# Performance work log

Hardware: AMD Instinct MI355X
Metric: run time of the kernel (lower is better)

Reference implementation:

```python
import jax, jax.numpy as jnp
import numpy as np

B, S, D, H = 4, 2048, 1024, 16
HD = D // H
QMIN, QMAX = -128.0, 127.0


def fq(x):
    """Int8 per-tensor fake-quant (quantize-dequantize), straight-through."""
    s = jnp.maximum(jnp.max(jnp.abs(x)) / QMAX, 1e-8)
    q = jnp.clip(jnp.round(x / s), QMIN, QMAX) * s
    return x + jax.lax.stop_gradient(q - x)


def layernorm(x, g, b):
    m = jnp.mean(x, axis=-1, keepdims=True)
    v = jnp.var(x, axis=-1, keepdims=True)
    return (x - m) * jax.lax.rsqrt(v + 1e-5) * g + b


def rope(x):
    # x: [B, H, S, HD]; rotate-half RoPE
    half = HD // 2
    inv = 1.0 / (10000.0 ** (jnp.arange(half, dtype=jnp.float32) / half))
    ang = jnp.arange(S, dtype=jnp.float32)[:, None] * inv[None, :]  # [S, half]
    cos, sin = jnp.cos(ang), jnp.sin(ang)
    x1, x2 = x[..., :half], x[..., half:]
    return jnp.concatenate([x1 * cos - x2 * sin, x1 * sin + x2 * cos], axis=-1)


def setup_inputs() -> dict:
    key = jax.random.key(0)
    ks = jax.random.split(key, 16)
    w = lambda k, shp: jax.random.normal(k, shp, dtype=jnp.float32) * 0.02
    return {
        "x": jax.random.normal(ks[0], (B, S, D), dtype=jnp.float32),
        "g1": jnp.ones((D,), jnp.float32), "bn1": jnp.zeros((D,), jnp.float32),
        "Wq": w(ks[1], (D, D)), "bq": jnp.zeros((D,), jnp.float32),
        "Wk": w(ks[2], (D, D)), "bk": jnp.zeros((D,), jnp.float32),
        "Wv": w(ks[3], (D, D)), "bv": jnp.zeros((D,), jnp.float32),
        "Wo": w(ks[4], (D, D)), "bo": jnp.zeros((D,), jnp.float32),
        "g2": jnp.ones((D,), jnp.float32), "bn2": jnp.zeros((D,), jnp.float32),
        "W1": w(ks[5], (4 * D, D)), "bf1": jnp.zeros((4 * D,), jnp.float32),
        "W2": w(ks[6], (D, 4 * D)), "bf2": jnp.zeros((D,), jnp.float32),
    }


def reference(x, g1, bn1, Wq, bq, Wk, bk, Wv, bv, Wo, bo, g2, bn2, W1, bf1, W2, bf2):
    # --- attention branch: LN -> int8 quant -> RoPE MHSA -> quant add ---
    residual = x
    h = fq(layernorm(x, g1, bn1))  # post_norm1_quant
    q = h @ fq(Wq).T + bq
    k = h @ fq(Wk).T + bk
    v = h @ fq(Wv).T + bv
    q = rope(q.reshape(B, S, H, HD).transpose(0, 2, 1, 3))
    k = rope(k.reshape(B, S, H, HD).transpose(0, 2, 1, 3))
    v = v.reshape(B, S, H, HD).transpose(0, 2, 1, 3)
    scores = jnp.einsum("bhqd,bhkd->bhqk", q, k) / np.sqrt(HD).astype(np.float32)
    attn = jax.nn.softmax(scores, axis=-1)
    o = jnp.einsum("bhqk,bhkd->bhqd", attn, v)
    o = o.transpose(0, 2, 1, 3).reshape(B, S, D)
    o = fq(o @ fq(Wo).T + bo)  # attn returns quant tensor
    x = fq(o + residual)       # QuantAdd
    # --- MLP branch: LN -> quant -> fc1 -> GELU -> quant -> fc2 -> quant add ---
    residual = x
    h = fq(layernorm(x, g2, bn2))  # post_norm2_quant
    h = h @ fq(W1).T + bf1
    h = jax.nn.gelu(h, approximate=False)
    h = fq(h)                       # post_gelu_quant
    h = h @ fq(W2).T + bf2
    return fq(h + residual)         # QuantAdd
```

## Files before the change

### kernel.cpp

```cpp
#include <hip/hip_runtime.h>
#include <math.h>

#define Bdim 4
#define Sdim 2048
#define Ddim 1024
#define Hdim 16
#define HDdim 64

typedef unsigned long long u64;
typedef unsigned short ushort_t;
typedef int int4v __attribute__((ext_vector_type(4)));
typedef short short8v __attribute__((ext_vector_type(8)));
typedef float float4v __attribute__((ext_vector_type(4)));
typedef unsigned short us4v __attribute__((ext_vector_type(4)));

__device__ __forceinline__ float qdq_f(float x, float amax) {
  float s = fmaxf(amax / 127.0f, 1e-8f);
  float r = rintf(x / s);
  r = fminf(fmaxf(r, -128.0f), 127.0f);
  return r * s;
}

__device__ __forceinline__ void atomicMaxF(float* a, float v) {
  atomicMax((int*)a, __float_as_int(v));
}

__device__ __forceinline__ float blockMax256(float v) {
  __shared__ float sred[4];
  #pragma unroll
  for (int o = 32; o > 0; o >>= 1) v = fmaxf(v, __shfl_xor(v, o));
  if ((threadIdx.x & 63) == 0) sred[threadIdx.x >> 6] = v;
  __syncthreads();
  return fmaxf(fmaxf(sred[0], sred[1]), fmaxf(sred[2], sred[3]));
}

__device__ __forceinline__ ushort_t f2bf(float f) {
  unsigned u = __float_as_uint(f);
  return (ushort_t)((u + 0x7FFFu + ((u >> 16) & 1u)) >> 16);
}
__device__ __forceinline__ float bf2f(ushort_t h) {
  return __uint_as_float(((unsigned)h) << 16);
}

__global__ void init_scalars(float* s) { s[threadIdx.x] = 0.0f; }

__global__ void bcat_kernel(const float* __restrict__ bq, const float* __restrict__ bk,
                            const float* __restrict__ bv, float* __restrict__ o) {
  int t = blockIdx.x * 256 + threadIdx.x;
  o[t] = (t < 1024) ? bq[t] : (t < 2048) ? bk[t - 1024] : bv[t - 2048];
}

__global__ __launch_bounds__(256) void absmax6_kernel(
    const float* __restrict__ Wq, const float* __restrict__ Wk,
    const float* __restrict__ Wv, const float* __restrict__ Wo,
    const float* __restrict__ W1, const float* __restrict__ W2,
    float* __restrict__ Sc)
{
  const u64 DD = (u64)Ddim * Ddim;
  int blk = blockIdx.x;
  const float* src; float* dst; u64 lb, nb, n;
  if (blk < 256)       { src = Wq; dst = Sc + 1; lb = blk;        nb = 256;  n = DD; }
  else if (blk < 512)  { src = Wk; dst = Sc + 2; lb = blk - 256;  nb = 256;  n = DD; }
  else if (blk < 768)  { src = Wv; dst = Sc + 3; lb = blk - 512;  nb = 256;  n = DD; }
  else if (blk < 1024) { src = Wo; dst = Sc + 4; lb = blk - 768;  nb = 256;  n = DD; }
  else if (blk < 2048) { src = W1; dst = Sc + 5; lb = blk - 1024; nb = 1024; n = 4 * DD; }
  else                 { src = W2; dst = Sc + 6; lb = blk - 2048; nb = 1024; n = 4 * DD; }
  u64 i = lb * 256 + threadIdx.x;
  u64 stride = nb * 256;
  float m = 0.0f;
  for (; i < n; i += stride) m = fmaxf(m, fabsf(src[i]));
  m = blockMax256(m);
  if (threadIdx.x == 0) atomicMaxF(dst, m);
}

__global__ __launch_bounds__(256) void quantw_kernel(
    const float* __restrict__ Wq, const float* __restrict__ Wk,
    const float* __restrict__ Wv, const float* __restrict__ Wo,
    const float* __restrict__ W1, const float* __restrict__ W2,
    signed char* __restrict__ Wq8, signed char* __restrict__ Wk8,
    signed char* __restrict__ Wv8, ushort_t* __restrict__ WoBF,
    signed char* __restrict__ W18, signed char* __restrict__ W28,
    const float* __restrict__ Sc)
{
  const u64 DD = (u64)Ddim * Ddim;
  int blk = blockIdx.x;
  if (blk < 2816) {
    const float* src; signed char* dst; float sa; u64 lb, nb, n4;
    if (blk < 256)       { src = Wq; dst = Wq8; sa = Sc[1]; lb = blk;        nb = 256;  n4 = DD / 4; }
    else if (blk < 512)  { src = Wk; dst = Wk8; sa = Sc[2]; lb = blk - 256;  nb = 256;  n4 = DD / 4; }
    else if (blk < 768)  { src = Wv; dst = Wv8; sa = Sc[3]; lb = blk - 512;  nb = 256;  n4 = DD / 4; }
    else if (blk < 1792) { src = W1; dst = W18; sa = Sc[5]; lb = blk - 768;  nb = 1024; n4 = DD; }
    else                 { src = W2; dst = W28; sa = Sc[6]; lb = blk - 1792; nb = 1024; n4 = DD; }
    const float is = 1.0f / fmaxf(sa / 127.0f, 1e-8f);
    u64 i = lb * 256 + threadIdx.x;
    u64 stride = nb * 256;
    for (; i < n4; i += stride) {
      float4 v = ((const float4*)src)[i];
      int b0 = (int)fminf(fmaxf(rintf(v.x * is), -128.0f), 127.0f) & 255;
      int b1 = (int)fminf(fmaxf(rintf(v.y * is), -128.0f), 127.0f) & 255;
      int b2 = (int)fminf(fmaxf(rintf(v.z * is), -128.0f), 127.0f) & 255;
      int b3 = (int)fminf(fmaxf(rintf(v.w * is), -128.0f), 127.0f) & 255;
      ((unsigned*)dst)[i] = (unsigned)(b0 | (b1 << 8) | (b2 << 16) | (b3 << 24));
    }
  } else {
    const float is = 1.0f / fmaxf(Sc[4] / 127.0f, 1e-8f);
    u64 i = (u64)(blk - 2816) * 256 + threadIdx.x;
    u64 stride = 1024ull * 256;
    for (; i < DD; i += stride) {
      float r = fminf(fmaxf(rintf(Wo[i] * is), -128.0f), 127.0f);
      WoBF[i] = f2bf(r);
    }
  }
}

__global__ __launch_bounds__(256) void quant8_kernel(
    const float* __restrict__ x, const float* __restrict__ amaxp,
    signed char* __restrict__ q, u64 n4)
{
  const float is = 1.0f / fmaxf(*amaxp / 127.0f, 1e-8f);
  u64 i = (u64)blockIdx.x * 256 + threadIdx.x;
  u64 stride = (u64)gridDim.x * 256;
  for (; i < n4; i += stride) {
    float4 v = ((const float4*)x)[i];
    int b0 = (int)fminf(fmaxf(rintf(v.x * is), -128.0f), 127.0f) & 255;
    int b1 = (int)fminf(fmaxf(rintf(v.y * is), -128.0f), 127.0f) & 255;
    int b2 = (int)fminf(fmaxf(rintf(v.z * is), -128.0f), 127.0f) & 255;
    int b3 = (int)fminf(fmaxf(rintf(v.w * is), -128.0f), 127.0f) & 255;
    ((unsigned*)q)[i] = (unsigned)(b0 | (b1 << 8) | (b2 << 16) | (b3 << 24));
  }
}

__global__ __launch_bounds__(256) void ln_kernel(
    const float* __restrict__ x, const float* __restrict__ g,
    const float* __restrict__ beta, const float* __restrict__ inAmax,
    float* __restrict__ y, float* __restrict__ amaxOut)
{
  __shared__ float sred[4];
  __shared__ float smv[2];
  const int tid = threadIdx.x;
  const u64 row = blockIdx.x;
  const float* xr = x + row * Ddim;
  float* yr = y + row * Ddim;
  float aIn = inAmax ? *inAmax : 0.0f;

  float vals[4];
  float sum = 0.0f;
  #pragma unroll
  for (int i = 0; i < 4; i++) {
    float v = xr[tid + (i << 8)];
    if (inAmax) v = qdq_f(v, aIn);
    vals[i] = v;
    sum += v;
  }
  #pragma unroll
  for (int o = 32; o > 0; o >>= 1) sum += __shfl_xor(sum, o);
  if ((tid & 63) == 0) sred[tid >> 6] = sum;
  __syncthreads();
  if (tid == 0) smv[0] = (sred[0] + sred[1] + sred[2] + sred[3]) * (1.0f / 1024.0f);
  __syncthreads();
  const float mean = smv[0];

  float dev = 0.0f;
  #pragma unroll
  for (int i = 0; i < 4; i++) { float d = vals[i] - mean; dev += d * d; }
  #pragma unroll
  for (int o = 32; o > 0; o >>= 1) dev += __shfl_xor(dev, o);
  if ((tid & 63) == 0) sred[tid >> 6] = dev;
  __syncthreads();
  if (tid == 0) {
    float var = (sred[0] + sred[1] + sred[2] + sred[3]) * (1.0f / 1024.0f);
    smv[1] = 1.0f / sqrtf(var + 1e-5f);
  }
  __syncthreads();
  const float inv = smv[1];

  float lmax = 0.0f;
  #pragma unroll
  for (int i = 0; i < 4; i++) {
    int c = tid + (i << 8);
    float ov = (vals[i] - mean) * inv * g[c] + beta[c];
    yr[c] = ov;
    lmax = fmaxf(lmax, fabsf(ov));
  }
  #pragma unroll
  for (int o = 32; o > 0; o >>= 1) lmax = fmaxf(lmax, __shfl_xor(lmax, o));
  __syncthreads();
  if ((tid & 63) == 0) sred[tid >> 6] = lmax;
  __syncthreads();
  if (tid == 0)
    atomicMaxF(amaxOut, fmaxf(fmaxf(sred[0], sred[1]), fmaxf(sred[2], sred[3])));
}

template <int EPI>
__global__ __launch_bounds__(256) void gemm_i8(
    const signed char* __restrict__ A8, const signed char* __restrict__ B8,
    const float* __restrict__ bias, float* __restrict__ C,
    int M, int N, int K,
    const float* __restrict__ sAp, const float* __restrict__ sBp,
    float* __restrict__ amaxOut,
    const float* __restrict__ Tm = nullptr,
    const float* __restrict__ amaxT = nullptr)
{
  __shared__ __align__(16) signed char As[128][80];
  __shared__ __align__(16) signed char Bs[128][80];
  const int tid = threadIdx.x;
  const int wave = tid >> 6, lane = tid & 63;
  const int quad = lane >> 4, l16 = lane & 15;
  const int wy = wave >> 1, wx = wave & 1;
  const int m0 = blockIdx.y << 7, n0 = blockIdx.x << 7;
  const float sA = fmaxf(*sAp / 127.0f, 1e-8f);
  const float sB = fmaxf(*sBp / 127.0f, 1e-8f);
  const float sAB = sA * sB;
  const float aT = (EPI == 2) ? *amaxT : 0.0f;

  const int sr = tid >> 2;
  const int sc = (tid & 3) << 4;

  int4v acc[4][4] = {};
  for (int k0 = 0; k0 < K; k0 += 64) {
    #pragma unroll
    for (int p = 0; p < 2; p++) {
      int r = sr + (p << 6);
      uint4 av = *(const uint4*)&A8[(u64)(m0 + r) * K + k0 + sc];
      uint4 bv = *(const uint4*)&B8[(u64)(n0 + r) * K + k0 + sc];
      *(uint4*)&As[r][sc] = av;
      *(uint4*)&Bs[r][sc] = bv;
    }
    __syncthreads();
    int4v af[4], bf[4];
    #pragma unroll
    for (int mt = 0; mt < 4; mt++)
      af[mt] = *(const int4v*)&As[(wy << 6) + (mt << 4) + l16][quad << 4];
    #pragma unroll
    for (int nt = 0; nt < 4; nt++)
      bf[nt] = *(const int4v*)&Bs[(wx << 6) + (nt << 4) + l16][quad << 4];
    #pragma unroll
    for (int mt = 0; mt < 4; mt++)
      #pragma unroll
      for (int nt = 0; nt < 4; nt++)
        acc[mt][nt] = __builtin_amdgcn_mfma_i32_16x16x64_i8(af[mt], bf[nt], acc[mt][nt], 0, 0, 0);
    __syncthreads();
  }

  float lmax = 0.0f;
  #pragma unroll
  for (int mt = 0; mt < 4; mt++) {
    #pragma unroll
    for (int reg = 0; reg < 4; reg++) {
      int row = m0 + (wy << 6) + (mt << 4) + (quad << 2) + reg;
      #pragma unroll
      for (int nt = 0; nt < 4; nt++) {
        int col = n0 + (wx << 6) + (nt << 4) + l16;
        float v = (float)acc[mt][nt][reg] * sAB + bias[col];
        if (EPI == 1) {
          v = 0.5f * v * (1.0f + erff(v * 0.70710678118654752440f));
          lmax = fmaxf(lmax, fabsf(v));
        }
        if (EPI == 2) {
          v += qdq_f(Tm[(u64)row * N + col], aT);
          lmax = fmaxf(lmax, fabsf(v));
        }
        C[(u64)row * N + col] = v;
      }
    }
  }
  if (EPI >= 1) {
    lmax = blockMax256(lmax);
    if (tid == 0) atomicMaxF(amaxOut, lmax);
  }
}

__global__ __launch_bounds__(256) void gemm_qkv3(
    const signed char* __restrict__ A8, const signed char* __restrict__ B8,
    const float* __restrict__ bias, float* __restrict__ C,
    const float* __restrict__ Sc)
{
  __shared__ __align__(16) signed char As[128][80];
  __shared__ __align__(16) signed char Bs[128][80];
  const int tid = threadIdx.x;
  const int wave = tid >> 6, lane = tid & 63;
  const int quad = lane >> 4, l16 = lane & 15;
  const int wy = wave >> 1, wx = wave & 1;
  const int m0 = blockIdx.y << 7, n0 = blockIdx.x << 7;
  const int K = Ddim, N = 3 * Ddim;
  const int seg = n0 >> 10;
  const float sA = fmaxf(Sc[0] / 127.0f, 1e-8f);
  const float sB = fmaxf(Sc[1 + seg] / 127.0f, 1e-8f);
  const float sAB = sA * sB;

  const int sr = tid >> 2;
  const int sc_ = (tid & 3) << 4;

  int4v acc[4][4] = {};
  for (int k0 = 0; k0 < K; k0 += 64) {
    #pragma unroll
    for (int p = 0; p < 2; p++) {
      int r = sr + (p << 6);
      uint4 av = *(const uint4*)&A8[(u64)(m0 + r) * K + k0 + sc_];
      uint4 bv = *(const uint4*)&B8[(u64)(n0 + r) * K + k0 + sc_];
      *(uint4*)&As[r][sc_] = av;
      *(uint4*)&Bs[r][sc_] = bv;
    }
    __syncthreads();
    int4v af[4], bf[4];
    #pragma unroll
    for (int mt = 0; mt < 4; mt++)
      af[mt] = *(const int4v*)&As[(wy << 6) + (mt << 4) + l16][quad << 4];
    #pragma unroll
    for (int nt = 0; nt < 4; nt++)
      bf[nt] = *(const int4v*)&Bs[(wx << 6) + (nt << 4) + l16][quad << 4];
    #pragma unroll
    for (int mt = 0; mt < 4; mt++)
      #pragma unroll
      for (int nt = 0; nt < 4; nt++)
        acc[mt][nt] = __builtin_amdgcn_mfma_i32_16x16x64_i8(af[mt], bf[nt], acc[mt][nt], 0, 0, 0);
    __syncthreads();
  }

  #pragma unroll
  for (int mt = 0; mt < 4; mt++) {
    #pragma unroll
    for (int reg = 0; reg < 4; reg++) {
      int row = m0 + (wy << 6) + (mt << 4) + (quad << 2) + reg;
      #pragma unroll
      for (int nt = 0; nt < 4; nt++) {
        int col = n0 + (wx << 6) + (nt << 4) + l16;
        C[(u64)row * N + col] = (float)acc[mt][nt][reg] * sAB + bias[col];
      }
    }
  }
}

__global__ __launch_bounds__(256) void gemm_bf16_wo(
    const ushort_t* __restrict__ Ahi, const ushort_t* __restrict__ Alo,
    const ushort_t* __restrict__ Bw, const float* __restrict__ bias,
    float* __restrict__ C, int M, int N, int K,
    const float* __restrict__ sWp, float* __restrict__ amaxOut)
{
  __shared__ __align__(16) ushort_t Hs[128][40];
  __shared__ __align__(16) ushort_t Ls[128][40];
  __shared__ __align__(16) ushort_t Ws[128][40];
  const int tid = threadIdx.x;
  const int wave = tid >> 6, lane = tid & 63;
  const int quad = lane >> 4, l16 = lane & 15;
  const int wy = wave >> 1, wx = wave & 1;
  const int m0 = blockIdx.y << 7, n0 = blockIdx.x << 7;
  const float sW = fmaxf(*sWp / 127.0f, 1e-8f);

  const int sr = tid >> 2;
  const int sce = (tid & 3) << 3;

  float4v acc[4][4] = {};
  for (int k0 = 0; k0 < K; k0 += 32) {
    #pragma unroll
    for (int p = 0; p < 2; p++) {
      int r = sr + (p << 6);
      uint4 hv = *(const uint4*)&Ahi[(u64)(m0 + r) * K + k0 + sce];
      uint4 lv = *(const uint4*)&Alo[(u64)(m0 + r) * K + k0 + sce];
      uint4 wv = *(const uint4*)&Bw[(u64)(n0 + r) * K + k0 + sce];
      *(uint4*)&Hs[r][sce] = hv;
      *(uint4*)&Ls[r][sce] = lv;
      *(uint4*)&Ws[r][sce] = wv;
    }
    __syncthreads();
    short8v ah[4], al[4], bw[4];
    #pragma unroll
    for (int mt = 0; mt < 4; mt++) {
      ah[mt] = *(const short8v*)&Hs[(wy << 6) + (mt << 4) + l16][quad << 3];
      al[mt] = *(const short8v*)&Ls[(wy << 6) + (mt << 4) + l16][quad << 3];
    }
    #pragma unroll
    for (int nt = 0; nt < 4; nt++)
      bw[nt] = *(const short8v*)&Ws[(wx << 6) + (nt << 4) + l16][quad << 3];
    #pragma unroll
    for (int mt = 0; mt < 4; mt++)
      #pragma unroll
      for (int nt = 0; nt < 4; nt++) {
        acc[mt][nt] = __builtin_amdgcn_mfma_f32_16x16x32_bf16(ah[mt], bw[nt], acc[mt][nt], 0, 0, 0);
        acc[mt][nt] = __builtin_amdgcn_mfma_f32_16x16x32_bf16(al[mt], bw[nt], acc[mt][nt], 0, 0, 0);
      }
    __syncthreads();
  }

  float lmax = 0.0f;
  #pragma unroll
  for (int mt = 0; mt < 4; mt++) {
    #pragma unroll
    for (int reg = 0; reg < 4; reg++) {
      int row = m0 + (wy << 6) + (mt << 4) + (quad << 2) + reg;
      #pragma unroll
      for (int nt = 0; nt < 4; nt++) {
        int col = n0 + (wx << 6) + (nt << 4) + l16;
        float v = acc[mt][nt][reg] * sW + bias[col];
        lmax = fmaxf(lmax, fabsf(v));
        C[(u64)row * N + col] = v;
      }
    }
  }
  lmax = blockMax256(lmax);
  if (tid == 0) atomicMaxF(amaxOut, lmax);
}

__global__ __launch_bounds__(256) void prep_attn(
    const float* __restrict__ QKV,
    ushort_t* __restrict__ QH, ushort_t* __restrict__ QL,
    ushort_t* __restrict__ KH, ushort_t* __restrict__ KL,
    ushort_t* __restrict__ VTH, ushort_t* __restrict__ VTL,
    float* __restrict__ NQ, float* __restrict__ KMX)
{
  const int bh = blockIdx.y;
  const int b = bh >> 4, h = bh & 15;
  const int s0 = blockIdx.x << 6;
  const int tid = threadIdx.x;
  float kml = 0.0f;

  #pragma unroll
  for (int i = 0; i < 8; i++) {
    int idx = tid + (i << 8);
    int s = idx >> 5, hp = idx & 31;
    int sa = s0 + s;
    u64 gin = (u64)(b * Sdim + sa) * 3072 + (h << 6) + hp;
    float inv = powf(10000.0f, -(float)hp * (1.0f / 32.0f));
    float ang = (float)sa * inv;
    float cs = cosf(ang), sn = sinf(ang);
    float q1 = QKV[gin],        q2 = QKV[gin + 32];
    float k1 = QKV[gin + 1024], k2 = QKV[gin + 1056];
    float qo1 = (q1 * cs - q2 * sn) * 0.125f;
    float qo2 = (q1 * sn + q2 * cs) * 0.125f;
    float ko1 = k1 * cs - k2 * sn;
    float ko2 = k1 * sn + k2 * cs;
    u64 go = ((u64)bh * Sdim + sa) * HDdim + hp;
    ushort_t t;
    t = f2bf(qo1); QH[go]      = t; QL[go]      = f2bf(qo1 - bf2f(t));
    t = f2bf(qo2); QH[go + 32] = t; QL[go + 32] = f2bf(qo2 - bf2f(t));
    t = f2bf(ko1); KH[go]      = t; KL[go]      = f2bf(ko1 - bf2f(t));
    t = f2bf(ko2); KH[go + 32] = t; KL[go + 32] = f2bf(ko2 - bf2f(t));
    float nq2 = qo1 * qo1 + qo2 * qo2;
    float nk2 = ko1 * ko1 + ko2 * ko2;
    #pragma unroll
    for (int o = 16; o >= 1; o >>= 1) {
      nq2 += __shfl_xor(nq2, o);
      nk2 += __shfl_xor(nk2, o);
    }
    if (hp == 0) {
      NQ[(u64)bh * Sdim + sa] = sqrtf(nq2);
      kml = fmaxf(kml, sqrtf(nk2));
    }
  }
  kml = blockMax256(kml);
  if (tid == 0) atomicMaxF(&KMX[bh], kml);

  __shared__ ushort_t VHs[64][66], VLs[64][66];
  #pragma unroll
  for (int i = 0; i < 4; i++) {
    int idx4 = tid + (i << 8);
    int s = idx4 >> 4, c4 = (idx4 & 15) << 2;
    u64 gin = (u64)(b * Sdim + s0 + s) * 3072 + 2048 + (h << 6) + c4;
    float4 vv = *(const float4*)&QKV[gin];
    float va[4] = {vv.x, vv.y, vv.z, vv.w};
    #pragma unroll
    for (int j = 0; j < 4; j++) {
      ushort_t vh = f2bf(va[j]);
      VHs[s][c4 + j] = vh;
      VLs[s][c4 + j] = f2bf(va[j] - bf2f(vh));
    }
  }
  __syncthreads();
  #pragma unroll
  for (int i = 0; i < 4; i++) {
    int idx4 = tid + (i << 8);
    int hd = idx4 >> 4, s4 = (idx4 & 15) << 2;
    us4v oh, ol;
    #pragma unroll
    for (int j = 0; j < 4; j++) { oh[j] = VHs[s4 + j][hd]; ol[j] = VLs[s4 + j][hd]; }
    u64 go = ((u64)bh * HDdim + hd) * Sdim + s0 + s4;
    *(us4v*)&VTH[go] = oh;
    *(us4v*)&VTL[go] = ol;
  }
}

__global__ __launch_bounds__(256) void attn_kernel(
    const ushort_t* __restrict__ QH, const ushort_t* __restrict__ QL,
    const ushort_t* __restrict__ KH, const ushort_t* __restrict__ KL,
    const ushort_t* __restrict__ VTH, const ushort_t* __restrict__ VTL,
    const float* __restrict__ NQ, const float* __restrict__ KMX,
    ushort_t* __restrict__ OHI, ushort_t* __restrict__ OLO)
{
  __shared__ __align__(16) ushort_t KHs[64][72], KLs[64][72];
  __shared__ __align__(16) ushort_t VHs[64][72], VLs[64][72];
  __shared__ __align__(16) float PF[128][68];
  const int tid = threadIdx.x;
  const int wave = tid >> 6, lane = tid & 63;
  const int quad = lane >> 4, l16 = lane & 15;
  const int w32 = wave << 5;
  const int bh = blockIdx.y;
  const int b = bh >> 4, h = bh & 15;
  const int q0 = blockIdx.x << 7;
  const u64 bhS = (u64)bh * Sdim;

  short8v qh[2][2], ql[2][2];
  #pragma unroll
  for (int mt = 0; mt < 2; mt++)
    #pragma unroll
    for (int kk = 0; kk < 2; kk++) {
      u64 g = (bhS + q0 + w32 + (mt << 4) + l16) * HDdim + (kk << 5) + (quad << 3);
      qh[mt][kk] = *(const short8v*)&QH[g];
      ql[mt][kk] = *(const short8v*)&QL[g];
    }

  const float kmax = KMX[bh] * 1.0009765625f;
  float Mb[2][4], lsum[2][4];
  #pragma unroll
  for (int mt = 0; mt < 2; mt++)
    #pragma unroll
    for (int r = 0; r < 4; r++) {
      Mb[mt][r] = NQ[bhS + q0 + w32 + (mt << 4) + (quad << 2) + r] * kmax;
      lsum[mt][r] = 0.0f;
    }

  float4v oacc[2][4] = {};

  for (int j0 = 0; j0 < Sdim; j0 += 64) {
    __syncthreads();
    #pragma unroll
    for (int i = 0; i < 2; i++) {
      int idx = tid + (i << 8);
      int r = idx >> 3, c8 = (idx & 7) << 3;
      u64 gk = (bhS + j0 + r) * HDdim + c8;
      *(uint4*)&KHs[r][c8] = *(const uint4*)&KH[gk];
      *(uint4*)&KLs[r][c8] = *(const uint4*)&KL[gk];
      u64 gv = ((u64)bh * HDdim + r) * Sdim + j0 + c8;
      *(uint4*)&VHs[r][c8] = *(const uint4*)&VTH[gv];
      *(uint4*)&VLs[r][c8] = *(const uint4*)&VTL[gv];
    }
    __syncthreads();

    float4v sc[2][4] = {};
    #pragma unroll
    for (int kk = 0; kk < 2; kk++)
      #pragma unroll
      for (int nt = 0; nt < 4; nt++) {
        short8v bh_ = *(const short8v*)&KHs[(nt << 4) + l16][(kk << 5) + (quad << 3)];
        short8v bl_ = *(const short8v*)&KLs[(nt << 4) + l16][(kk << 5) + (quad << 3)];
        #pragma unroll
        for (int mt = 0; mt < 2; mt++) {
          sc[mt][nt] = __builtin_amdgcn_mfma_f32_16x16x32_bf16(qh[mt][kk], bh_, sc[mt][nt], 0, 0, 0);
          sc[mt][nt] = __builtin_amdgcn_mfma_f32_16x16x32_bf16(qh[mt][kk], bl_, sc[mt][nt], 0, 0, 0);
          sc[mt][nt] = __builtin_amdgcn_mfma_f32_16x16x32_bf16(ql[mt][kk], bh_, sc[mt][nt], 0, 0, 0);
        }
      }

    #pragma unroll
    for (int mt = 0; mt < 2; mt++)
      #pragma unroll
      for (int r = 0; r < 4; r++) {
        int prow = w32 + (mt << 4) + (quad << 2) + r;
        float lacc = 0.0f;
        #pragma unroll
        for (int nt = 0; nt < 4; nt++) {
          float p = __expf(sc[mt][nt][r] - Mb[mt][r]);
          lacc += p;
          PF[prow][(nt << 4) + l16] = p;
        }
        lsum[mt][r] += lacc;
      }

    #pragma unroll
    for (int kk = 0; kk < 2; kk++) {
      short8v vh[4], vl[4];
      #pragma unroll
      for (int nt = 0; nt < 4; nt++) {
        vh[nt] = *(const short8v*)&VHs[(nt << 4) + l16][(kk << 5) + (quad << 3)];
        vl[nt] = *(const short8v*)&VLs[(nt << 4) + l16][(kk << 5) + (quad << 3)];
      }
      #pragma unroll
      for (int mt = 0; mt < 2; mt++) {
        const float* prp = &PF[w32 + (mt << 4) + l16][(kk << 5) + (quad << 3)];
        float4v pa = *(const float4v*)prp;
        float4v pb = *(const float4v*)(prp + 4);
        short8v ph, pl;
        #pragma unroll
        for (int j = 0; j < 4; j++) {
          unsigned ua = __float_as_uint(pa[j]);
          unsigned ub = __float_as_uint(pb[j]);
          float la = pa[j] - __uint_as_float(ua & 0xffff0000u);
          float lb = pb[j] - __uint_as_float(ub & 0xffff0000u);
          ph[j]     = (short)(ua >> 16);
          ph[4 + j] = (short)(ub >> 16);
          pl[j]     = (short)(__float_as_uint(la) >> 16);
          pl[4 + j] = (short)(__float_as_uint(lb) >> 16);
        }
        #pragma unroll
        for (int nt = 0; nt < 4; nt++) {
          oacc[mt][nt] = __builtin_amdgcn_mfma_f32_16x16x32_bf16(ph, vh[nt], oacc[mt][nt], 0, 0, 0);
          oacc[mt][nt] = __builtin_amdgcn_mfma_f32_16x16x32_bf16(ph, vl[nt], oacc[mt][nt], 0, 0, 0);
          oacc[mt][nt] = __builtin_amdgcn_mfma_f32_16x16x32_bf16(pl, vh[nt], oacc[mt][nt], 0, 0, 0);
        }
      }
    }
  }

  #pragma unroll
  for (int mt = 0; mt < 2; mt++)
    #pragma unroll
    for (int r = 0; r < 4; r++) {
      float l = lsum[mt][r];
      #pragma unroll
      for (int o = 8; o >= 1; o >>= 1) l += __shfl_xor(l, o);
      lsum[mt][r] = l;
    }

  #pragma unroll
  for (int mt = 0; mt < 2; mt++)
    #pragma unroll
    for (int r = 0; r < 4; r++) {
      float invl = 1.0f / lsum[mt][r];
      int srow = q0 + w32 + (mt << 4) + (quad << 2) + r;
      u64 gbase = ((u64)(b * Sdim + srow) * Hdim + h) * HDdim;
      #pragma unroll
      for (int nt = 0; nt < 4; nt++) {
        float o = oacc[mt][nt][r] * invl;
        ushort_t t = f2bf(o);
        OHI[gbase + (nt << 4) + l16] = t;
        OLO[gbase + (nt << 4) + l16] = f2bf(o - bf2f(t));
      }
    }
}

__global__ __launch_bounds__(256) void add_qdq_kernel(
    const float* __restrict__ a, const float* __restrict__ amaxA,
    const float* __restrict__ x, float* __restrict__ outp, u64 n,
    float* __restrict__ amaxOut)
{
  const float aA = *amaxA;
  u64 i = (u64)blockIdx.x * 256 + threadIdx.x;
  u64 stride = (u64)gridDim.x * 256;
  float m = 0.0f;
  for (; i < n; i += stride) {
    float t = qdq_f(a[i], aA) + x[i];
    outp[i] = t;
    m = fmaxf(m, fabsf(t));
  }
  m = blockMax256(m);
  if (threadIdx.x == 0) atomicMaxF(amaxOut, m);
}

__global__ __launch_bounds__(256) void qdq_out_kernel(
    const float* __restrict__ u, const float* __restrict__ amaxU,
    float* __restrict__ o, u64 n)
{
  const float aU = *amaxU;
  u64 i = (u64)blockIdx.x * 256 + threadIdx.x;
  u64 stride = (u64)gridDim.x * 256;
  for (; i < n; i += stride) o[i] = qdq_f(u[i], aU);
}

extern "C" void kernel_launch(void* const* d_in, const int* in_sizes, int n_in,
                              void* d_out, int out_size, void* d_ws, size_t ws_size,
                              hipStream_t stream)
{
  const float* x   = (const float*)d_in[0];
  const float* g1  = (const float*)d_in[1];
  const float* bn1 = (const float*)d_in[2];
  const float* Wq  = (const float*)d_in[3];
  const float* bq  = (const float*)d_in[4];
  const float* Wk  = (const float*)d_in[5];
  const float* bk  = (const float*)d_in[6];
  const float* Wv  = (const float*)d_in[7];
  const float* bv  = (const float*)d_in[8];
  const float* Wo  = (const float*)d_in[9];
  const float* bo  = (const float*)d_in[10];
  const float* g2  = (const float*)d_in[11];
  const float* bn2 = (const float*)d_in[12];
  const float* W1  = (const float*)d_in[13];
  const float* bf1 = (const float*)d_in[14];
  const float* W2  = (const float*)d_in[15];
  const float* bf2 = (const float*)d_in[16];
  float* out = (float*)d_out;

  const u64 NBSD = (u64)Bdim * Sdim * Ddim;
  const u64 NB4  = NBSD * 4;
  const u64 DD   = (u64)Ddim * Ddim;

  char* Wb = (char*)d_ws;
  float*       Sc   = (float*)Wb;
  float*       U0   = (float*)(Wb + 1024);
  float*       U1   = (float*)(Wb + 1024 + NB4);
  float*       F    = (float*)(Wb + 1024 + 2 * NB4);
  signed char* A8   = (signed char*)(Wb + 1024 + 6 * NB4);
  signed char* Wq8  = A8 + NBSD;
  signed char* Wk8  = Wq8 + DD;
  signed char* Wv8  = Wk8 + DD;
  signed char* W18  = Wv8 + DD;
  signed char* W28  = W18 + 4 * DD;
  ushort_t*    WoBF = (ushort_t*)(W28 + 4 * DD);
  float*       NQ   = (float*)(WoBF + DD);
  float*       BQKV = NQ + (u64)64 * Sdim;
  float*       KMX  = Sc + 128;

  float* QKV = U1;
  float* F0  = F;
  ushort_t* QHp = (ushort_t*)(F + 2 * NBSD);
  ushort_t* QLp = QHp + NBSD;
  ushort_t* KHp = (ushort_t*)(F + 3 * NBSD);
  ushort_t* KLp = KHp + NBSD;
  ushort_t* VTH = (ushort_t*)U0;
  ushort_t* VTL = VTH + NBSD;
  ushort_t* OHI = (ushort_t*)U1;
  ushort_t* OLO = OHI + NBSD;
  signed char* G8 = (signed char*)U0;

  const u64 needBytes = (u64)((char*)(BQKV + 3072) - Wb);
  if (ws_size < needBytes) return;

  init_scalars<<<1, 256, 0, stream>>>(Sc);
  bcat_kernel<<<12, 256, 0, stream>>>(bq, bk, bv, BQKV);

  ln_kernel<<<Bdim * Sdim, 256, 0, stream>>>(x, g1, bn1, nullptr, U0, Sc + 0);

  absmax6_kernel<<<3072, 256, 0, stream>>>(Wq, Wk, Wv, Wo, W1, W2, Sc);

  quant8_kernel<<<4096, 256, 0, stream>>>(U0, Sc + 0, A8, NBSD / 4);
  quantw_kernel<<<3840, 256, 0, stream>>>(Wq, Wk, Wv, Wo, W1, W2,
                                          Wq8, Wk8, Wv8, WoBF, W18, W28, Sc);

  const int M = Bdim * Sdim;

  dim3 gQKV(3 * Ddim / 128, M / 128);
  gemm_qkv3<<<gQKV, 256, 0, stream>>>(A8, Wq8, BQKV, QKV, Sc);

  dim3 gPrep(Sdim / 64, Bdim * Hdim);
  prep_attn<<<gPrep, 256, 0, stream>>>(QKV, QHp, QLp, KHp, KLp, VTH, VTL, NQ, KMX);

  dim3 gAttn(Sdim / 128, Bdim * Hdim);
  attn_kernel<<<gAttn, 256, 0, stream>>>(QHp, QLp, KHp, KLp, VTH, VTL, NQ, KMX, OHI, OLO);

  dim3 gP(Ddim / 128, M / 128);
  gemm_bf16_wo<<<gP, 256, 0, stream>>>(OHI, OLO, WoBF, bo, F0, M, Ddim, Ddim, Sc + 4, Sc + 7);

  add_qdq_kernel<<<4096, 256, 0, stream>>>(F0, Sc + 7, x, U1, NBSD, Sc + 8);

  ln_kernel<<<Bdim * Sdim, 256, 0, stream>>>(U1, g2, bn2, Sc + 8, U0, Sc + 9);
  quant8_kernel<<<4096, 256, 0, stream>>>(U0, Sc + 9, A8, NBSD / 4);

  dim3 gF1(4 * Ddim / 128, M / 128);
  gemm_i8<1><<<gF1, 256, 0, stream>>>(A8, W18, bf1, F, M, 4 * Ddim, Ddim, Sc + 9, Sc + 5, Sc + 10);

  quant8_kernel<<<4096, 256, 0, stream>>>(F, Sc + 10, G8, NBSD);

  gemm_i8<2><<<gP, 256, 0, stream>>>(G8, W28, bf2, out, M, Ddim, 4 * Ddim,
                                     Sc + 10, Sc + 6, Sc + 11, U1, Sc + 8);

  qdq_out_kernel<<<4096, 256, 0, stream>>>(out, Sc + 11, out, NBSD);
}
```

Before: 1.075 ms.

## Enlarge attention query tile to 256 rows with 32-key steps; merge init kernels

The attention kernel now gives each wave 64 query rows instead of 32, so each block covers 256 queries, and it steps over keys 32 at a time with smaller shared-memory tiles. Each K/V tile loaded from global memory is reused across twice as many queries, which halves K/V traffic per query and raises MFMA density per LDS load. In exchange the register use for Q fragments and accumulators doubles, the grid shrinks to 512 blocks, and there are twice as many loop iterations and barriers. Separately, the scalar-init and bias-concat kernels are merged into one launch.

```diff
diff --git a/kernel.cpp b/kernel.cpp
--- a/kernel.cpp
+++ b/kernel.cpp
@@ -42,11 +42,11 @@
   return __uint_as_float(((unsigned)h) << 16);
 }
 
-__global__ void init_scalars(float* s) { s[threadIdx.x] = 0.0f; }
-
-__global__ void bcat_kernel(const float* __restrict__ bq, const float* __restrict__ bk,
+__global__ void init_kernel(float* __restrict__ s,
+                            const float* __restrict__ bq, const float* __restrict__ bk,
                             const float* __restrict__ bv, float* __restrict__ o) {
-  int t = blockIdx.x * 256 + threadIdx.x;
+  if (blockIdx.x == 0) { s[threadIdx.x] = 0.0f; return; }
+  int t = (blockIdx.x - 1) * 256 + threadIdx.x;
   o[t] = (t < 1024) ? bq[t] : (t < 2048) ? bk[t - 1024] : bv[t - 2048];
 }
 
@@ -486,122 +486,119 @@
     const float* __restrict__ NQ, const float* __restrict__ KMX,
     ushort_t* __restrict__ OHI, ushort_t* __restrict__ OLO)
 {
-  __shared__ __align__(16) ushort_t KHs[64][72], KLs[64][72];
-  __shared__ __align__(16) ushort_t VHs[64][72], VLs[64][72];
-  __shared__ __align__(16) float PF[128][68];
+  __shared__ __align__(16) ushort_t KHs[32][72], KLs[32][72];
+  __shared__ __align__(16) ushort_t VHs[64][40], VLs[64][40];
+  __shared__ __align__(16) float PF[256][36];
   const int tid = threadIdx.x;
   const int wave = tid >> 6, lane = tid & 63;
   const int quad = lane >> 4, l16 = lane & 15;
-  const int w32 = wave << 5;
+  const int w64 = wave << 6;
   const int bh = blockIdx.y;
   const int b = bh >> 4, h = bh & 15;
-  const int q0 = blockIdx.x << 7;
+  const int q0 = blockIdx.x << 8;
   const u64 bhS = (u64)bh * Sdim;
 
-  short8v qh[2][2], ql[2][2];
-  #pragma unroll
-  for (int mt = 0; mt < 2; mt++)
+  short8v qh[4][2], ql[4][2];
+  #pragma unroll
+  for (int mt = 0; mt < 4; mt++)
     #pragma unroll
     for (int kk = 0; kk < 2; kk++) {
-      u64 g = (bhS + q0 + w32 + (mt << 4) + l16) * HDdim + (kk << 5) + (quad << 3);
+      u64 g = (bhS + q0 + w64 + (mt << 4) + l16) * HDdim + (kk << 5) + (quad << 3);
       qh[mt][kk] = *(const short8v*)&QH[g];
       ql[mt][kk] = *(const short8v*)&QL[g];
     }
 
   const float kmax = KMX[bh] * 1.0009765625f;
-  float Mb[2][4], lsum[2][4];
-  #pragma unroll
-  for (int mt = 0; mt < 2; mt++)
+  float Mb[4][4], lsum[4][4];
+  #pragma unroll
+  for (int mt = 0; mt < 4; mt++)
     #pragma unroll
     for (int r = 0; r < 4; r++) {
-      Mb[mt][r] = NQ[bhS + q0 + w32 + (mt << 4) + (quad << 2) + r] * kmax;
+      Mb[mt][r] = NQ[bhS + q0 + w64 + (mt << 4) + (quad << 2) + r] * kmax;
       lsum[mt][r] = 0.0f;
     }
 
-  float4v oacc[2][4] = {};
-
-  for (int j0 = 0; j0 < Sdim; j0 += 64) {
+  float4v oacc[4][4] = {};
+
+  for (int j0 = 0; j0 < Sdim; j0 += 32) {
     __syncthreads();
-    #pragma unroll
-    for (int i = 0; i < 2; i++) {
-      int idx = tid + (i << 8);
-      int r = idx >> 3, c8 = (idx & 7) << 3;
+    {
+      int r = tid >> 3, c8 = (tid & 7) << 3;
       u64 gk = (bhS + j0 + r) * HDdim + c8;
       *(uint4*)&KHs[r][c8] = *(const uint4*)&KH[gk];
       *(uint4*)&KLs[r][c8] = *(const uint4*)&KL[gk];
-      u64 gv = ((u64)bh * HDdim + r) * Sdim + j0 + c8;
-      *(uint4*)&VHs[r][c8] = *(const uint4*)&VTH[gv];
-      *(uint4*)&VLs[r][c8] = *(const uint4*)&VTL[gv];
+      int r2 = tid >> 2, c82 = (tid & 3) << 3;
+      u64 gv = ((u64)bh * HDdim + r2) * Sdim + j0 + c82;
+      *(uint4*)&VHs[r2][c82] = *(const uint4*)&VTH[gv];
+      *(uint4*)&VLs[r2][c82] = *(const uint4*)&VTL[gv];
     }
     __syncthreads();
 
-    float4v sc[2][4] = {};
-    #pragma unroll
-    for (int kk = 0; kk < 2; kk++)
+    float4v sc[4][2] = {};
+    #pragma unroll
+    for (int kk = 0; kk < 2; kk++) {
+      short8v kf_h[2], kf_l[2];
+      #pragma unroll
+      for (int nt = 0; nt < 2; nt++) {
+        kf_h[nt] = *(const short8v*)&KHs[(nt << 4) + l16][(kk << 5) + (quad << 3)];
+        kf_l[nt] = *(const short8v*)&KLs[(nt << 4) + l16][(kk << 5) + (quad << 3)];
+      }
+      #pragma unroll
+      for (int mt = 0; mt < 4; mt++)
+        #pragma unroll
+        for (int nt = 0; nt < 2; nt++) {
+          sc[mt][nt] = __builtin_amdgcn_mfma_f32_16x16x32_bf16(qh[mt][kk], kf_h[nt], sc[mt][nt], 0, 0, 0);
+          sc[mt][nt] = __builtin_amdgcn_mfma_f32_16x16x32_bf16(qh[mt][kk], kf_l[nt], sc[mt][nt], 0, 0, 0);
+          sc[mt][nt] = __builtin_amdgcn_mfma_f32_16x16x32_bf16(ql[mt][kk], kf_h[nt], sc[mt][nt], 0, 0, 0);
+        }
+    }
+
+    #pragma unroll
+    for (int mt = 0; mt < 4; mt++)
+      #pragma unroll
+      for (int r = 0; r < 4; r++) {
+        int prow = w64 + (mt << 4) + (quad << 2) + r;
+        float p0 = __expf(sc[mt][0][r] - Mb[mt][r]);
+        float p1 = __expf(sc[mt][1][r] - Mb[mt][r]);
+        PF[prow][l16] = p0;
+        PF[prow][16 + l16] = p1;
+        lsum[mt][r] += p0 + p1;
+      }
+
+    short8v vh[4], vl[4];
+    #pragma unroll
+    for (int nt = 0; nt < 4; nt++) {
+      vh[nt] = *(const short8v*)&VHs[(nt << 4) + l16][quad << 3];
+      vl[nt] = *(const short8v*)&VLs[(nt << 4) + l16][quad << 3];
+    }
+    #pragma unroll
+    for (int mt = 0; mt < 4; mt++) {
+      const float* prp = &PF[w64 + (mt << 4) + l16][quad << 3];
+      float4v pa = *(const float4v*)prp;
+      float4v pb = *(const float4v*)(prp + 4);
+      short8v ph, pl;
+      #pragma unroll
+      for (int j = 0; j < 4; j++) {
+        unsigned ua = __float_as_uint(pa[j]);
+        unsigned ub = __float_as_uint(pb[j]);
+        float la = pa[j] - __uint_as_float(ua & 0xffff0000u);
+        float lb = pb[j] - __uint_as_float(ub & 0xffff0000u);
+        ph[j]     = (short)(ua >> 16);
+        ph[4 + j] = (short)(ub >> 16);
+        pl[j]     = (short)(__float_as_uint(la) >> 16);
+        pl[4 + j] = (short)(__float_as_uint(lb) >> 16);
+      }
       #pragma unroll
       for (int nt = 0; nt < 4; nt++) {
-        short8v bh_ = *(const short8v*)&KHs[(nt << 4) + l16][(kk << 5) + (quad << 3)];
-        short8v bl_ = *(const short8v*)&KLs[(nt << 4) + l16][(kk << 5) + (quad << 3)];
-        #pragma unroll
-        for (int mt = 0; mt < 2; mt++) {
-          sc[mt][nt] = __builtin_amdgcn_mfma_f32_16x16x32_bf16(qh[mt][kk], bh_, sc[mt][nt], 0, 0, 0);
-          sc[mt][nt] = __builtin_amdgcn_mfma_f32_16x16x32_bf16(qh[mt][kk], bl_, sc[mt][nt], 0, 0, 0);
-          sc[mt][nt] = __builtin_amdgcn_mfma_f32_16x16x32_bf16(ql[mt][kk], bh_, sc[mt][nt], 0, 0, 0);
-        }
-      }
-
-    #pragma unroll
-    for (int mt = 0; mt < 2; mt++)
-      #pragma unroll
-      for (int r = 0; r < 4; r++) {
-        int prow = w32 + (mt << 4) + (quad << 2) + r;
-        float lacc = 0.0f;
-        #pragma unroll
-        for (int nt = 0; nt < 4; nt++) {
-          float p = __expf(sc[mt][nt][r] - Mb[mt][r]);
-          lacc += p;
-          PF[prow][(nt << 4) + l16] = p;
-        }
-        lsum[mt][r] += lacc;
-      }
-
-    #pragma unroll
-    for (int kk = 0; kk < 2; kk++) {
-      short8v vh[4], vl[4];
-      #pragma unroll
-      for (int nt = 0; nt < 4; nt++) {
-        vh[nt] = *(const short8v*)&VHs[(nt << 4) + l16][(kk << 5) + (quad << 3)];
-        vl[nt] = *(const short8v*)&VLs[(nt << 4) + l16][(kk << 5) + (quad << 3)];
-      }
-      #pragma unroll
-      for (int mt = 0; mt < 2; mt++) {
-        const float* prp = &PF[w32 + (mt << 4) + l16][(kk << 5) + (quad << 3)];
-        float4v pa = *(const float4v*)prp;
-        float4v pb = *(const float4v*)(prp + 4);
-        short8v ph, pl;
-        #pragma unroll
-        for (int j = 0; j < 4; j++) {
-          unsigned ua = __float_as_uint(pa[j]);
-          unsigned ub = __float_as_uint(pb[j]);
-          float la = pa[j] - __uint_as_float(ua & 0xffff0000u);
-          float lb = pb[j] - __uint_as_float(ub & 0xffff0000u);
-          ph[j]     = (short)(ua >> 16);
-          ph[4 + j] = (short)(ub >> 16);
-          pl[j]     = (short)(__float_as_uint(la) >> 16);
-          pl[4 + j] = (short)(__float_as_uint(lb) >> 16);
-        }
-        #pragma unroll
-        for (int nt = 0; nt < 4; nt++) {
-          oacc[mt][nt] = __builtin_amdgcn_mfma_f32_16x16x32_bf16(ph, vh[nt], oacc[mt][nt], 0, 0, 0);
-          oacc[mt][nt] = __builtin_amdgcn_mfma_f32_16x16x32_bf16(ph, vl[nt], oacc[mt][nt], 0, 0, 0);
-          oacc[mt][nt] = __builtin_amdgcn_mfma_f32_16x16x32_bf16(pl, vh[nt], oacc[mt][nt], 0, 0, 0);
-        }
-      }
-    }
-  }
-
-  #pragma unroll
-  for (int mt = 0; mt < 2; mt++)
+        oacc[mt][nt] = __builtin_amdgcn_mfma_f32_16x16x32_bf16(ph, vh[nt], oacc[mt][nt], 0, 0, 0);
+        oacc[mt][nt] = __builtin_amdgcn_mfma_f32_16x16x32_bf16(ph, vl[nt], oacc[mt][nt], 0, 0, 0);
+        oacc[mt][nt] = __builtin_amdgcn_mfma_f32_16x16x32_bf16(pl, vh[nt], oacc[mt][nt], 0, 0, 0);
+      }
+    }
+  }
+
+  #pragma unroll
+  for (int mt = 0; mt < 4; mt++)
     #pragma unroll
     for (int r = 0; r < 4; r++) {
       float l = lsum[mt][r];
@@ -611,11 +608,11 @@
     }
 
   #pragma unroll
-  for (int mt = 0; mt < 2; mt++)
+  for (int mt = 0; mt < 4; mt++)
     #pragma unroll
     for (int r = 0; r < 4; r++) {
       float invl = 1.0f / lsum[mt][r];
-      int srow = q0 + w32 + (mt << 4) + (quad << 2) + r;
+      int srow = q0 + w64 + (mt << 4) + (quad << 2) + r;
       u64 gbase = ((u64)(b * Sdim + srow) * Hdim + h) * HDdim;
       #pragma unroll
       for (int nt = 0; nt < 4; nt++) {
@@ -713,8 +710,7 @@
   const u64 needBytes = (u64)((char*)(BQKV + 3072) - Wb);
   if (ws_size < needBytes) return;
 
-  init_scalars<<<1, 256, 0, stream>>>(Sc);
-  bcat_kernel<<<12, 256, 0, stream>>>(bq, bk, bv, BQKV);
+  init_kernel<<<13, 256, 0, stream>>>(Sc, bq, bk, bv, BQKV);
 
   ln_kernel<<<Bdim * Sdim, 256, 0, stream>>>(x, g1, bn1, nullptr, U0, Sc + 0);
 
@@ -732,7 +728,7 @@
   dim3 gPrep(Sdim / 64, Bdim * Hdim);
   prep_attn<<<gPrep, 256, 0, stream>>>(QKV, QHp, QLp, KHp, KLp, VTH, VTL, NQ, KMX);
 
-  dim3 gAttn(Sdim / 128, Bdim * Hdim);
+  dim3 gAttn(Sdim / 256, Bdim * Hdim);
   attn_kernel<<<gAttn, 256, 0, stream>>>(QHp, QLp, KHp, KLp, VTH, VTL, NQ, KMX, OHI, OLO);
 
   dim3 gP(Ddim / 128, M / 128);
```

Result: slower. 1.129 ms (+5.0%).
